# Optimization experiments

Measured on AMD Instinct MI355X. Metric: run time of the kernel, lower is better.

Reference implementation:

```python
import jax, jax.numpy as jnp
import numpy as np
from jax import lax

H = W = 1024

def _conv_sig(x, w, b):
    # 3x3 conv, padding=1 (SAME), NCHW / OIHW, followed by sigmoid
    y = lax.conv_general_dilated(x, w, (1, 1), 'SAME',
                                 dimension_numbers=('NCHW', 'OIHW', 'NCHW'))
    return jax.nn.sigmoid(y + b[None, :, None, None])


def setup_inputs() -> dict:
    key = jax.random.key(0)
    ks = jax.random.split(key, 20)
    d = {
        'x':  jax.random.normal(ks[0], (1, 3, H, W), jnp.float32),
        'x2': jax.random.normal(ks[1], (1, 3, H, W), jnp.float32),
        'w1a': jax.random.normal(ks[2], (1, 3, 3, 3), jnp.float32) * 0.1,
        'b1a': jax.random.normal(ks[3], (1,), jnp.float32) * 0.1,
        'w2a': jax.random.normal(ks[4], (1, 4, 3, 3), jnp.float32) * 0.1,
        'b2a': jax.random.normal(ks[5], (1,), jnp.float32) * 0.1,
        'w3a': jax.random.normal(ks[6], (1, 5, 3, 3), jnp.float32) * 0.1,
        'b3a': jax.random.normal(ks[7], (1,), jnp.float32) * 0.1,
        'w1b': jax.random.normal(ks[8], (1, 3, 3, 3), jnp.float32) * 0.1,
        'b1b': jax.random.normal(ks[9], (1,), jnp.float32) * 0.1,
        'w2b': jax.random.normal(ks[10], (1, 4, 3, 3), jnp.float32) * 0.1,
        'b2b': jax.random.normal(ks[11], (1,), jnp.float32) * 0.1,
        'w3b': jax.random.normal(ks[12], (1, 5, 3, 3), jnp.float32) * 0.1,
        'b3b': jax.random.normal(ks[13], (1,), jnp.float32) * 0.1,
        'lw1': jax.random.normal(ks[14], (128, 6), jnp.float32) * 0.1,
        'lb1': jax.random.normal(ks[15], (128,), jnp.float32) * 0.1,
        'lw2': jax.random.normal(ks[16], (2, 128), jnp.float32) * 0.1,
        'lb2': jax.random.normal(ks[17], (2,), jnp.float32) * 0.1,
    }
    return d


def _encode(x, params):
    # three stacked conv(3x3)+sigmoid blocks with densenet-style concat: C 3->4->5->6
    (w1, b1), (w2, b2), (w3, b3) = params
    x = jnp.concatenate([x, _conv_sig(x, w1, b1)], axis=1)
    x = jnp.concatenate([x, _conv_sig(x, w2, b2)], axis=1)
    x = jnp.concatenate([x, _conv_sig(x, w3, b3)], axis=1)
    return x  # [1, 6, H, W]


def reference(x, x2, w1a, b1a, w2a, b2a, w3a, b3a,
              w1b, b1b, w2b, b2b, w3b, b3b, lw1, lb1, lw2, lb2):
    # name branch: passthrough (3-channel input, e.g. name='opt')
    xa = _encode(x,  [(w1a, b1a), (w2a, b2a), (w3a, b3a)])
    xb = _encode(x2, [(w1b, b1b), (w2b, b2b), (w3b, b3b)])
    x3 = xa - xb                                   # [1, 6, H, W]
    feat = jnp.transpose(x3, (0, 2, 3, 1)).reshape(H * W, 6)
    feat = feat @ lw1.T + lb1                      # [HW, 128]
    outfeature = feat @ lw2.T + lb2                # [HW, 2]
    den_x1 = jnp.transpose(xa, (0, 2, 3, 1)).reshape(H, W, 6)
    den_x2 = jnp.transpose(xb, (0, 2, 3, 1)).reshape(H, W, 6)
    return outfeature, den_x1, den_x2
```

## Files before the change

### kernel.cpp

```cpp
#include <hip/hip_runtime.h>
#include <math.h>

#define IMG  1024
#define TS   32
#define HALO 3
#define XT   38
#define S1T  36
#define S2T  34

__device__ __forceinline__ float sigf(float y) {
    return 1.0f / (1.0f + __expf(-y));
}

__device__ __forceinline__ void acc9(float acc[4], const float v[6][3], const float* w9) {
#pragma unroll
    for (int dy = 0; dy < 3; ++dy)
#pragma unroll
        for (int dx = 0; dx < 3; ++dx) {
            float ww = w9[dy * 3 + dx];
#pragma unroll
            for (int rr = 0; rr < 4; ++rr)
                acc[rr] += ww * v[rr + dy][dx];
        }
}

__global__ void combine_lin(const float* __restrict__ lw1, const float* __restrict__ lb1,
                            const float* __restrict__ lw2, const float* __restrict__ lb2,
                            float* __restrict__ ws) {
    int t = threadIdx.x;
    if (t < 12) {
        int o = t / 6, c = t % 6;
        float acc = 0.0f;
        for (int k = 0; k < 128; ++k) acc += lw2[o * 128 + k] * lw1[k * 6 + c];
        ws[o * 6 + c] = acc;
    } else if (t < 14) {
        int o = t - 12;
        float acc = lb2[o];
        for (int k = 0; k < 128; ++k) acc += lw2[o * 128 + k] * lb1[k];
        ws[12 + o] = acc;
    }
}

__global__ __launch_bounds__(256, 2)
void unet_fused(const float* __restrict__ x, const float* __restrict__ x2,
                const float* __restrict__ w1a, const float* __restrict__ b1a,
                const float* __restrict__ w2a, const float* __restrict__ b2a,
                const float* __restrict__ w3a, const float* __restrict__ b3a,
                const float* __restrict__ w1b, const float* __restrict__ b1b,
                const float* __restrict__ w2b, const float* __restrict__ b2b,
                const float* __restrict__ w3b, const float* __restrict__ b3b,
                const float* __restrict__ wsc,
                float* __restrict__ out)
{
    __shared__ float xt[2][3][XT * XT];
    __shared__ float s1[2][S1T * S1T];
    __shared__ float s2[2][S2T * S2T];
    __shared__ float s3[2][TS * TS];

    const int tid = threadIdx.x;
    const int bx = blockIdx.x, by = blockIdx.y;
    const int row0 = by * TS - HALO, col0 = bx * TS - HALO;

    const float* W1[2] = {w1a, w1b};
    const float* W2[2] = {w2a, w2b};
    const float* W3[2] = {w3a, w3b};
    const float* B1[2] = {b1a, b1b};
    const float* B2[2] = {b2a, b2b};
    const float* B3[2] = {b3a, b3b};

    for (int idx = tid; idx < 3 * XT * XT; idx += 256) {
        int pl = idx / (XT * XT);
        int i  = idx - pl * (XT * XT);
        int r = i / XT, c = i - r * XT;
        int gr = row0 + r, gc = col0 + c;
        bool ok = ((unsigned)gr < (unsigned)IMG) && ((unsigned)gc < (unsigned)IMG);
        float v0 = 0.0f, v1 = 0.0f;
        if (ok) {
            long g = (long)pl * (IMG * IMG) + (long)gr * IMG + gc;
            v0 = x[g];
            v1 = x2[g];
        }
        xt[0][pl][i] = v0;
        xt[1][pl][i] = v1;
    }
    __syncthreads();

    for (int br = 0; br < 2; ++br) {
        float w[27];
#pragma unroll
        for (int i = 0; i < 27; ++i) w[i] = W1[br][i];
        const float bias = B1[br][0];
        for (int item = tid; item < S1T * 9; item += 256) {
            int c = item % S1T, rg = item / S1T;
            int r0 = rg * 4;
            float acc[4] = {bias, bias, bias, bias};
#pragma unroll
            for (int ic = 0; ic < 3; ++ic) {
                const float* xp = &xt[br][ic][r0 * XT + c];
                float v[6][3];
#pragma unroll
                for (int rr = 0; rr < 6; ++rr)
#pragma unroll
                    for (int cc = 0; cc < 3; ++cc)
                        v[rr][cc] = xp[rr * XT + cc];
                acc9(acc, v, &w[ic * 9]);
            }
            int gc1 = col0 + 1 + c;
            bool cok = (unsigned)gc1 < (unsigned)IMG;
            float* so = &s1[br][r0 * S1T + c];
#pragma unroll
            for (int rr = 0; rr < 4; ++rr) {
                int gr1 = row0 + 1 + r0 + rr;
                bool ok = cok && ((unsigned)gr1 < (unsigned)IMG);
                so[rr * S1T] = ok ? sigf(acc[rr]) : 0.0f;
            }
        }
    }
    __syncthreads();

    for (int br = 0; br < 2; ++br) {
        float w[36];
#pragma unroll
        for (int i = 0; i < 36; ++i) w[i] = W2[br][i];
        const float bias = B2[br][0];
        for (int item = tid; item < S2T * 9; item += 256) {
            int c = item % S2T, rg = item / S2T;
            int r0 = rg * 4;
            float acc[4] = {bias, bias, bias, bias};
#pragma unroll
            for (int ic = 0; ic < 3; ++ic) {
                float v[6][3];
#pragma unroll
                for (int rr = 0; rr < 6; ++rr) {
                    int rrow = r0 + 1 + rr; if (rrow > XT - 1) rrow = XT - 1;
#pragma unroll
                    for (int cc = 0; cc < 3; ++cc)
                        v[rr][cc] = xt[br][ic][rrow * XT + (c + 1 + cc)];
                }
                acc9(acc, v, &w[ic * 9]);
            }
            {
                float v[6][3];
#pragma unroll
                for (int rr = 0; rr < 6; ++rr) {
                    int rrow = r0 + rr; if (rrow > S1T - 1) rrow = S1T - 1;
#pragma unroll
                    for (int cc = 0; cc < 3; ++cc)
                        v[rr][cc] = s1[br][rrow * S1T + (c + cc)];
                }
                acc9(acc, v, &w[27]);
            }
            int gc2 = col0 + 2 + c;
            bool cok = (unsigned)gc2 < (unsigned)IMG;
            float* so = &s2[br][r0 * S2T + c];
#pragma unroll
            for (int rr = 0; rr < 4; ++rr) {
                int srow = r0 + rr;
                if (srow < S2T) {
                    int gr2 = row0 + 2 + srow;
                    bool ok = cok && ((unsigned)gr2 < (unsigned)IMG);
                    so[rr * S2T] = ok ? sigf(acc[rr]) : 0.0f;
                }
            }
        }
    }
    __syncthreads();

    for (int br = 0; br < 2; ++br) {
        float w[45];
#pragma unroll
        for (int i = 0; i < 45; ++i) w[i] = W3[br][i];
        const float bias = B3[br][0];
        {
            int item = tid;
            int c = item & 31, rg = item >> 5;
            int r0 = rg * 4;
            float acc[4] = {bias, bias, bias, bias};
#pragma unroll
            for (int ic = 0; ic < 3; ++ic) {
                float v[6][3];
#pragma unroll
                for (int rr = 0; rr < 6; ++rr)
#pragma unroll
                    for (int cc = 0; cc < 3; ++cc)
                        v[rr][cc] = xt[br][ic][(r0 + 2 + rr) * XT + (c + 2 + cc)];
                acc9(acc, v, &w[ic * 9]);
            }
            {
                float v[6][3];
#pragma unroll
                for (int rr = 0; rr < 6; ++rr)
#pragma unroll
                    for (int cc = 0; cc < 3; ++cc)
                        v[rr][cc] = s1[br][(r0 + 1 + rr) * S1T + (c + 1 + cc)];
                acc9(acc, v, &w[27]);
            }
            {
                float v[6][3];
#pragma unroll
                for (int rr = 0; rr < 6; ++rr)
#pragma unroll
                    for (int cc = 0; cc < 3; ++cc)
                        v[rr][cc] = s2[br][(r0 + rr) * S2T + (c + cc)];
                acc9(acc, v, &w[36]);
            }
            float* so = &s3[br][r0 * TS + c];
#pragma unroll
            for (int rr = 0; rr < 4; ++rr)
                so[rr * TS] = sigf(acc[rr]);
        }
    }
    __syncthreads();

    float wcr[14];
#pragma unroll
    for (int i = 0; i < 14; ++i) wcr[i] = wsc[i];
    const long out1 = (long)2 * IMG * IMG;
    const long out2 = out1 + (long)6 * IMG * IMG;
    for (int p = tid; p < TS * TS; p += 256) {
        int r = p >> 5, c = p & 31;
        long gr = (long)by * TS + r, gc = (long)bx * TS + c;
        long pix = gr * IMG + gc;
        float a[6], b[6];
#pragma unroll
        for (int ch = 0; ch < 3; ++ch) {
            a[ch] = xt[0][ch][(r + 3) * XT + (c + 3)];
            b[ch] = xt[1][ch][(r + 3) * XT + (c + 3)];
        }
        a[3] = s1[0][(r + 2) * S1T + (c + 2)];
        b[3] = s1[1][(r + 2) * S1T + (c + 2)];
        a[4] = s2[0][(r + 1) * S2T + (c + 1)];
        b[4] = s2[1][(r + 1) * S2T + (c + 1)];
        a[5] = s3[0][r * TS + c];
        b[5] = s3[1][r * TS + c];

        float* p1 = out + out1 + pix * 6;
        float* p2 = out + out2 + pix * 6;
#pragma unroll
        for (int ch = 0; ch < 6; ++ch) { p1[ch] = a[ch]; p2[ch] = b[ch]; }

        float o0 = wcr[12], o1 = wcr[13];
#pragma unroll
        for (int ch = 0; ch < 6; ++ch) {
            float d = a[ch] - b[ch];
            o0 += wcr[ch]     * d;
            o1 += wcr[6 + ch] * d;
        }
        out[pix * 2]     = o0;
        out[pix * 2 + 1] = o1;
    }
}

extern "C" void kernel_launch(void* const* d_in, const int* in_sizes, int n_in,
                              void* d_out, int out_size, void* d_ws, size_t ws_size,
                              hipStream_t stream) {
    const float* x   = (const float*)d_in[0];
    const float* x2  = (const float*)d_in[1];
    const float* w1a = (const float*)d_in[2];
    const float* b1a = (const float*)d_in[3];
    const float* w2a = (const float*)d_in[4];
    const float* b2a = (const float*)d_in[5];
    const float* w3a = (const float*)d_in[6];
    const float* b3a = (const float*)d_in[7];
    const float* w1b = (const float*)d_in[8];
    const float* b1b = (const float*)d_in[9];
    const float* w2b = (const float*)d_in[10];
    const float* b2b = (const float*)d_in[11];
    const float* w3b = (const float*)d_in[12];
    const float* b3b = (const float*)d_in[13];
    const float* lw1 = (const float*)d_in[14];
    const float* lb1 = (const float*)d_in[15];
    const float* lw2 = (const float*)d_in[16];
    const float* lb2 = (const float*)d_in[17];
    float* ws  = (float*)d_ws;
    float* out = (float*)d_out;

    combine_lin<<<1, 64, 0, stream>>>(lw1, lb1, lw2, lb2, ws);

    dim3 grid(IMG / TS, IMG / TS);
    unet_fused<<<grid, 256, 0, stream>>>(x, x2,
                                         w1a, b1a, w2a, b2a, w3a, b3a,
                                         w1b, b1b, w2b, b2b, w3b, b3b,
                                         ws, out);
}
```

Measured before the change: 162.0 us.

## Process branches sequentially to halve shared memory and fuse linear-weight combine

The kernel now runs the two encoder branches one after another, reusing a single set of shared-memory tiles, and drops the s3 tile by keeping the third conv output in registers. Branch A's features are kept in registers for the final linear projection. The separate combine_lin launch is folded into every block, and launch bounds are raised to allow more resident blocks. In exchange each block does more barriers, loads its inputs serially, recomputes the 128-length weight products redundantly per block, and holds more registers.

Measured after the change: 155.7 us. 1.04x faster.

```diff
diff --git a/kernel.cpp b/kernel.cpp
--- a/kernel.cpp
+++ b/kernel.cpp
@@ -24,24 +24,7 @@
         }
 }
 
-__global__ void combine_lin(const float* __restrict__ lw1, const float* __restrict__ lb1,
-                            const float* __restrict__ lw2, const float* __restrict__ lb2,
-                            float* __restrict__ ws) {
-    int t = threadIdx.x;
-    if (t < 12) {
-        int o = t / 6, c = t % 6;
-        float acc = 0.0f;
-        for (int k = 0; k < 128; ++k) acc += lw2[o * 128 + k] * lw1[k * 6 + c];
-        ws[o * 6 + c] = acc;
-    } else if (t < 14) {
-        int o = t - 12;
-        float acc = lb2[o];
-        for (int k = 0; k < 128; ++k) acc += lw2[o * 128 + k] * lb1[k];
-        ws[12 + o] = acc;
-    }
-}
-
-__global__ __launch_bounds__(256, 2)
+__global__ __launch_bounds__(256, 4)
 void unet_fused(const float* __restrict__ x, const float* __restrict__ x2,
                 const float* __restrict__ w1a, const float* __restrict__ b1a,
                 const float* __restrict__ w2a, const float* __restrict__ b2a,
@@ -49,18 +32,35 @@
                 const float* __restrict__ w1b, const float* __restrict__ b1b,
                 const float* __restrict__ w2b, const float* __restrict__ b2b,
                 const float* __restrict__ w3b, const float* __restrict__ b3b,
-                const float* __restrict__ wsc,
+                const float* __restrict__ lw1, const float* __restrict__ lb1,
+                const float* __restrict__ lw2, const float* __restrict__ lb2,
                 float* __restrict__ out)
 {
-    __shared__ float xt[2][3][XT * XT];
-    __shared__ float s1[2][S1T * S1T];
-    __shared__ float s2[2][S2T * S2T];
-    __shared__ float s3[2][TS * TS];
+    __shared__ float xt[3][XT * XT];
+    __shared__ float s1[S1T * S1T];
+    __shared__ float s2[S2T * S2T];
+    __shared__ float wc[14];
 
     const int tid = threadIdx.x;
     const int bx = blockIdx.x, by = blockIdx.y;
     const int row0 = by * TS - HALO, col0 = bx * TS - HALO;
 
+    const int c_out = tid & 31;
+    const int r0_out = (tid >> 5) * 4;
+
+    if (tid < 12) {
+        int o = tid / 6, ch = tid % 6;
+        float acc = 0.0f;
+        for (int k = 0; k < 128; ++k) acc += lw2[o * 128 + k] * lw1[k * 6 + ch];
+        wc[tid] = acc;
+    } else if (tid < 14) {
+        int o = tid - 12;
+        float acc = lb2[o];
+        for (int k = 0; k < 128; ++k) acc += lw2[o * 128 + k] * lb1[k];
+        wc[tid] = acc;
+    }
+
+    const float* XS[2] = {x, x2};
     const float* W1[2] = {w1a, w1b};
     const float* W2[2] = {w2a, w2b};
     const float* W3[2] = {w3a, w3b};
@@ -68,123 +68,132 @@
     const float* B2[2] = {b2a, b2b};
     const float* B3[2] = {b3a, b3b};
 
-    for (int idx = tid; idx < 3 * XT * XT; idx += 256) {
-        int pl = idx / (XT * XT);
-        int i  = idx - pl * (XT * XT);
-        int r = i / XT, c = i - r * XT;
-        int gr = row0 + r, gc = col0 + c;
-        bool ok = ((unsigned)gr < (unsigned)IMG) && ((unsigned)gc < (unsigned)IMG);
-        float v0 = 0.0f, v1 = 0.0f;
-        if (ok) {
-            long g = (long)pl * (IMG * IMG) + (long)gr * IMG + gc;
-            v0 = x[g];
-            v1 = x2[g];
-        }
-        xt[0][pl][i] = v0;
-        xt[1][pl][i] = v1;
-    }
-    __syncthreads();
-
+    const long out1 = (long)2 * IMG * IMG;
+    const long out2 = out1 + (long)6 * IMG * IMG;
+
+    float areg[4][6];
+
+#pragma unroll
     for (int br = 0; br < 2; ++br) {
-        float w[27];
-#pragma unroll
-        for (int i = 0; i < 27; ++i) w[i] = W1[br][i];
-        const float bias = B1[br][0];
-        for (int item = tid; item < S1T * 9; item += 256) {
-            int c = item % S1T, rg = item / S1T;
-            int r0 = rg * 4;
-            float acc[4] = {bias, bias, bias, bias};
-#pragma unroll
-            for (int ic = 0; ic < 3; ++ic) {
-                const float* xp = &xt[br][ic][r0 * XT + c];
-                float v[6][3];
-#pragma unroll
-                for (int rr = 0; rr < 6; ++rr)
-#pragma unroll
-                    for (int cc = 0; cc < 3; ++cc)
-                        v[rr][cc] = xp[rr * XT + cc];
-                acc9(acc, v, &w[ic * 9]);
-            }
-            int gc1 = col0 + 1 + c;
-            bool cok = (unsigned)gc1 < (unsigned)IMG;
-            float* so = &s1[br][r0 * S1T + c];
-#pragma unroll
-            for (int rr = 0; rr < 4; ++rr) {
-                int gr1 = row0 + 1 + r0 + rr;
-                bool ok = cok && ((unsigned)gr1 < (unsigned)IMG);
-                so[rr * S1T] = ok ? sigf(acc[rr]) : 0.0f;
-            }
-        }
-    }
-    __syncthreads();
-
-    for (int br = 0; br < 2; ++br) {
-        float w[36];
-#pragma unroll
-        for (int i = 0; i < 36; ++i) w[i] = W2[br][i];
-        const float bias = B2[br][0];
-        for (int item = tid; item < S2T * 9; item += 256) {
-            int c = item % S2T, rg = item / S2T;
-            int r0 = rg * 4;
+        const float* xin = XS[br];
+        for (int idx = tid; idx < 3 * XT * XT; idx += 256) {
+            int pl = idx / (XT * XT);
+            int i  = idx - pl * (XT * XT);
+            int r = i / XT, cc = i - r * XT;
+            int gr = row0 + r, gc = col0 + cc;
+            bool ok = ((unsigned)gr < (unsigned)IMG) && ((unsigned)gc < (unsigned)IMG);
+            float v = 0.0f;
+            if (ok) v = xin[(long)pl * (IMG * IMG) + (long)gr * IMG + gc];
+            xt[pl][i] = v;
+        }
+        __syncthreads();
+
+        {
+            float w[27];
+#pragma unroll
+            for (int i = 0; i < 27; ++i) w[i] = W1[br][i];
+            const float bias = B1[br][0];
+            for (int item = tid; item < S1T * 9; item += 256) {
+                int c = item % S1T, rg = item / S1T;
+                int r0 = rg * 4;
+                float acc[4] = {bias, bias, bias, bias};
+#pragma unroll
+                for (int ic = 0; ic < 3; ++ic) {
+                    const float* xp = &xt[ic][r0 * XT + c];
+                    float v[6][3];
+#pragma unroll
+                    for (int rr = 0; rr < 6; ++rr)
+#pragma unroll
+                        for (int cc = 0; cc < 3; ++cc)
+                            v[rr][cc] = xp[rr * XT + cc];
+                    acc9(acc, v, &w[ic * 9]);
+                }
+                int gc1 = col0 + 1 + c;
+                bool cok = (unsigned)gc1 < (unsigned)IMG;
+                float* so = &s1[r0 * S1T + c];
+#pragma unroll
+                for (int rr = 0; rr < 4; ++rr) {
+                    int gr1 = row0 + 1 + r0 + rr;
+                    bool ok = cok && ((unsigned)gr1 < (unsigned)IMG);
+                    so[rr * S1T] = ok ? sigf(acc[rr]) : 0.0f;
+                }
+            }
+        }
+        __syncthreads();
+
+        {
+            float w[36];
+#pragma unroll
+            for (int i = 0; i < 36; ++i) w[i] = W2[br][i];
+            const float bias = B2[br][0];
+            for (int item = tid; item < S2T * 9; item += 256) {
+                int c = item % S2T, rg = item / S2T;
+                int r0 = rg * 4;
+                float acc[4] = {bias, bias, bias, bias};
+#pragma unroll
+                for (int ic = 0; ic < 3; ++ic) {
+                    float v[6][3];
+#pragma unroll
+                    for (int rr = 0; rr < 6; ++rr) {
+                        int rrow = r0 + 1 + rr; if (rrow > XT - 1) rrow = XT - 1;
+#pragma unroll
+                        for (int cc = 0; cc < 3; ++cc)
+                            v[rr][cc] = xt[ic][rrow * XT + (c + 1 + cc)];
+                    }
+                    acc9(acc, v, &w[ic * 9]);
+                }
+                {
+                    float v[6][3];
+#pragma unroll
+                    for (int rr = 0; rr < 6; ++rr) {
+                        int rrow = r0 + rr; if (rrow > S1T - 1) rrow = S1T - 1;
+#pragma unroll
+                        for (int cc = 0; cc < 3; ++cc)
+                            v[rr][cc] = s1[rrow * S1T + (c + cc)];
+                    }
+                    acc9(acc, v, &w[27]);
+                }
+                int gc2 = col0 + 2 + c;
+                bool cok = (unsigned)gc2 < (unsigned)IMG;
+                float* so = &s2[r0 * S2T + c];
+#pragma unroll
+                for (int rr = 0; rr < 4; ++rr) {
+                    int srow = r0 + rr;
+                    if (srow < S2T) {
+                        int gr2 = row0 + 2 + srow;
+                        bool ok = cok && ((unsigned)gr2 < (unsigned)IMG);
+                        so[rr * S2T] = ok ? sigf(acc[rr]) : 0.0f;
+                    }
+                }
+            }
+        }
+        __syncthreads();
+
+        {
+            float w[45];
+#pragma unroll
+            for (int i = 0; i < 45; ++i) w[i] = W3[br][i];
+            const float bias = B3[br][0];
+            const int c = c_out, r0 = r0_out;
             float acc[4] = {bias, bias, bias, bias};
 #pragma unroll
             for (int ic = 0; ic < 3; ++ic) {
                 float v[6][3];
 #pragma unroll
-                for (int rr = 0; rr < 6; ++rr) {
-                    int rrow = r0 + 1 + rr; if (rrow > XT - 1) rrow = XT - 1;
+                for (int rr = 0; rr < 6; ++rr)
 #pragma unroll
                     for (int cc = 0; cc < 3; ++cc)
-                        v[rr][cc] = xt[br][ic][rrow * XT + (c + 1 + cc)];
-                }
+                        v[rr][cc] = xt[ic][(r0 + 2 + rr) * XT + (c + 2 + cc)];
                 acc9(acc, v, &w[ic * 9]);
             }
             {
                 float v[6][3];
 #pragma unroll
-                for (int rr = 0; rr < 6; ++rr) {
-                    int rrow = r0 + rr; if (rrow > S1T - 1) rrow = S1T - 1;
+                for (int rr = 0; rr < 6; ++rr)
 #pragma unroll
                     for (int cc = 0; cc < 3; ++cc)
-                        v[rr][cc] = s1[br][rrow * S1T + (c + cc)];
-                }
+                        v[rr][cc] = s1[(r0 + 1 + rr) * S1T + (c + 1 + cc)];
                 acc9(acc, v, &w[27]);
-            }
-            int gc2 = col0 + 2 + c;
-            bool cok = (unsigned)gc2 < (unsigned)IMG;
-            float* so = &s2[br][r0 * S2T + c];
-#pragma unroll
-            for (int rr = 0; rr < 4; ++rr) {
-                int srow = r0 + rr;
-                if (srow < S2T) {
-                    int gr2 = row0 + 2 + srow;
-                    bool ok = cok && ((unsigned)gr2 < (unsigned)IMG);
-                    so[rr * S2T] = ok ? sigf(acc[rr]) : 0.0f;
-                }
-            }
-        }
-    }
-    __syncthreads();
-
-    for (int br = 0; br < 2; ++br) {
-        float w[45];
-#pragma unroll
-        for (int i = 0; i < 45; ++i) w[i] = W3[br][i];
-        const float bias = B3[br][0];
-        {
-            int item = tid;
-            int c = item & 31, rg = item >> 5;
-            int r0 = rg * 4;
-            float acc[4] = {bias, bias, bias, bias};
-#pragma unroll
-            for (int ic = 0; ic < 3; ++ic) {
-                float v[6][3];
-#pragma unroll
-                for (int rr = 0; rr < 6; ++rr)
-#pragma unroll
-                    for (int cc = 0; cc < 3; ++cc)
-                        v[rr][cc] = xt[br][ic][(r0 + 2 + rr) * XT + (c + 2 + cc)];
-                acc9(acc, v, &w[ic * 9]);
             }
             {
                 float v[6][3];
@@ -192,62 +201,57 @@
                 for (int rr = 0; rr < 6; ++rr)
 #pragma unroll
                     for (int cc = 0; cc < 3; ++cc)
-                        v[rr][cc] = s1[br][(r0 + 1 + rr) * S1T + (c + 1 + cc)];
-                acc9(acc, v, &w[27]);
-            }
-            {
-                float v[6][3];
-#pragma unroll
-                for (int rr = 0; rr < 6; ++rr)
-#pragma unroll
-                    for (int cc = 0; cc < 3; ++cc)
-                        v[rr][cc] = s2[br][(r0 + rr) * S2T + (c + cc)];
+                        v[rr][cc] = s2[(r0 + rr) * S2T + (c + cc)];
                 acc9(acc, v, &w[36]);
             }
-            float* so = &s3[br][r0 * TS + c];
-#pragma unroll
-            for (int rr = 0; rr < 4; ++rr)
-                so[rr * TS] = sigf(acc[rr]);
-        }
-    }
-    __syncthreads();
-
-    float wcr[14];
-#pragma unroll
-    for (int i = 0; i < 14; ++i) wcr[i] = wsc[i];
-    const long out1 = (long)2 * IMG * IMG;
-    const long out2 = out1 + (long)6 * IMG * IMG;
-    for (int p = tid; p < TS * TS; p += 256) {
-        int r = p >> 5, c = p & 31;
-        long gr = (long)by * TS + r, gc = (long)bx * TS + c;
-        long pix = gr * IMG + gc;
-        float a[6], b[6];
-#pragma unroll
-        for (int ch = 0; ch < 3; ++ch) {
-            a[ch] = xt[0][ch][(r + 3) * XT + (c + 3)];
-            b[ch] = xt[1][ch][(r + 3) * XT + (c + 3)];
-        }
-        a[3] = s1[0][(r + 2) * S1T + (c + 2)];
-        b[3] = s1[1][(r + 2) * S1T + (c + 2)];
-        a[4] = s2[0][(r + 1) * S2T + (c + 1)];
-        b[4] = s2[1][(r + 1) * S2T + (c + 1)];
-        a[5] = s3[0][r * TS + c];
-        b[5] = s3[1][r * TS + c];
-
-        float* p1 = out + out1 + pix * 6;
-        float* p2 = out + out2 + pix * 6;
-#pragma unroll
-        for (int ch = 0; ch < 6; ++ch) { p1[ch] = a[ch]; p2[ch] = b[ch]; }
-
-        float o0 = wcr[12], o1 = wcr[13];
-#pragma unroll
-        for (int ch = 0; ch < 6; ++ch) {
-            float d = a[ch] - b[ch];
-            o0 += wcr[ch]     * d;
-            o1 += wcr[6 + ch] * d;
-        }
-        out[pix * 2]     = o0;
-        out[pix * 2 + 1] = o1;
+
+            float cur[4][6];
+#pragma unroll
+            for (int rr = 0; rr < 4; ++rr) {
+#pragma unroll
+                for (int ch = 0; ch < 3; ++ch)
+                    cur[rr][ch] = xt[ch][(r0 + 3 + rr) * XT + (c + 3)];
+                cur[rr][3] = s1[(r0 + 2 + rr) * S1T + (c + 2)];
+                cur[rr][4] = s2[(r0 + 1 + rr) * S2T + (c + 1)];
+                cur[rr][5] = sigf(acc[rr]);
+            }
+
+            const long denOff = (br == 0) ? out1 : out2;
+#pragma unroll
+            for (int rr = 0; rr < 4; ++rr) {
+                long gr = (long)by * TS + r0 + rr;
+                long pix = gr * IMG + ((long)bx * TS + c);
+                float* pd = out + denOff + pix * 6;
+#pragma unroll
+                for (int ch = 0; ch < 6; ++ch) pd[ch] = cur[rr][ch];
+            }
+
+            if (br == 0) {
+#pragma unroll
+                for (int rr = 0; rr < 4; ++rr)
+#pragma unroll
+                    for (int ch = 0; ch < 6; ++ch) areg[rr][ch] = cur[rr][ch];
+            } else {
+                float wcr[14];
+#pragma unroll
+                for (int i = 0; i < 14; ++i) wcr[i] = wc[i];
+#pragma unroll
+                for (int rr = 0; rr < 4; ++rr) {
+                    float o0 = wcr[12], o1 = wcr[13];
+#pragma unroll
+                    for (int ch = 0; ch < 6; ++ch) {
+                        float d = areg[rr][ch] - cur[rr][ch];
+                        o0 += wcr[ch]     * d;
+                        o1 += wcr[6 + ch] * d;
+                    }
+                    long gr = (long)by * TS + r0 + rr;
+                    long pix = gr * IMG + ((long)bx * TS + c);
+                    out[pix * 2]     = o0;
+                    out[pix * 2 + 1] = o1;
+                }
+            }
+        }
+        __syncthreads();
     }
 }
 
@@ -272,14 +276,11 @@
     const float* lb1 = (const float*)d_in[15];
     const float* lw2 = (const float*)d_in[16];
     const float* lb2 = (const float*)d_in[17];
-    float* ws  = (float*)d_ws;
     float* out = (float*)d_out;
-
-    combine_lin<<<1, 64, 0, stream>>>(lw1, lb1, lw2, lb2, ws);
 
     dim3 grid(IMG / TS, IMG / TS);
     unet_fused<<<grid, 256, 0, stream>>>(x, x2,
                                          w1a, b1a, w2a, b2a, w3a, b3a,
                                          w1b, b1b, w2b, b2b, w3b, b3b,
-                                         ws, out);
-}
+                                         lw1, lb1, lw2, lb2, out);
+}
```
